# Performance work log

Measured on AMD Instinct MI355X. Metric: run time of the kernel, lower is better.

## Reference

```python
import jax, jax.numpy as jnp
import numpy as np

N_SEQ = 100_000
N_LAB = 64
E_CON = 1_600_000
D_IN = 128; D_HID = 128; BEL_OUT = 64; INC_OUT = 128
BN_EPS = 1e-5


def setup_inputs() -> dict:
    key = jax.random.key(0)
    ks = jax.random.split(key, 16)
    def W(k, i, o):
        return jax.random.normal(k, (i, o), jnp.float32) / np.float32(np.sqrt(i))
    return {
        "x_seq": jax.random.normal(ks[0], (N_SEQ, D_IN), jnp.float32),
        "x_label": jax.random.normal(ks[1], (N_LAB, D_IN), jnp.float32),
        "W1_bel": W(ks[2], D_IN, D_HID), "b1_bel": jnp.zeros((D_HID,), jnp.float32),
        "W1_inc": W(ks[3], D_IN, D_HID), "b1_inc": jnp.zeros((D_HID,), jnp.float32),
        "W1_con": W(ks[4], D_IN, D_HID), "b1_con": jnp.zeros((D_HID,), jnp.float32),
        "g1s": jnp.ones((D_HID,), jnp.float32), "beta1s": jnp.zeros((D_HID,), jnp.float32),
        "g1l": jnp.ones((D_HID,), jnp.float32), "beta1l": jnp.zeros((D_HID,), jnp.float32),
        "W2_bel": W(ks[5], D_HID, BEL_OUT), "b2_bel": jnp.zeros((BEL_OUT,), jnp.float32),
        "W2_inc": W(ks[6], D_HID, INC_OUT), "b2_inc": jnp.zeros((INC_OUT,), jnp.float32),
        "W2_con": W(ks[7], D_HID, INC_OUT), "b2_con": jnp.zeros((INC_OUT,), jnp.float32),
        "g2s": jnp.ones((INC_OUT,), jnp.float32), "beta2s": jnp.zeros((INC_OUT,), jnp.float32),
        "g2l": jnp.ones((BEL_OUT,), jnp.float32), "beta2l": jnp.zeros((BEL_OUT,), jnp.float32),
        "bel_label": jax.random.randint(ks[8], (N_SEQ,), 0, N_LAB),
        "con_src": jax.random.randint(ks[9], (E_CON,), 0, N_SEQ),
        "con_dst": jax.random.randint(ks[10], (E_CON,), 0, N_SEQ),
    }


def _inv_sqrt_deg(deg):
    # DGL norm='both': deg^{-1/2}, zero-degree nodes get 0
    return jnp.where(deg > 0, jax.lax.rsqrt(jnp.maximum(deg, 1.0)), 0.0)


def _gconv(x_src, src, dst, n_dst, W, b):
    # DGL GraphConv: y = D_dst^{-1/2} A D_src^{-1/2} x W + b
    n_src = x_src.shape[0]
    ones = jnp.ones(src.shape, x_src.dtype)
    deg_out = jax.ops.segment_sum(ones, src, num_segments=n_src)
    deg_in = jax.ops.segment_sum(ones, dst, num_segments=n_dst)
    xs = x_src * _inv_sqrt_deg(deg_out)[:, None]
    agg = jax.ops.segment_sum(xs[src], dst, num_segments=n_dst)  # [n_dst, d]
    agg = agg * _inv_sqrt_deg(deg_in)[:, None]
    return agg @ W + b


def _bn(x, g, b):
    # BatchNorm1d, training mode: biased variance, eps=1e-5
    m = jnp.mean(x, axis=0)
    v = jnp.mean(jnp.square(x - m), axis=0)
    return (x - m) * jax.lax.rsqrt(v + BN_EPS) * g + b


def _hetero_layer(h_seq, h_lab, bel_label, con_src, con_dst, Wb, bb, Wi, bi, Wc, bc):
    seq_idx = jnp.arange(h_seq.shape[0])
    # belongs_to: sequence -> label
    lab = _gconv(h_seq, seq_idx, bel_label, h_lab.shape[0], Wb, bb)
    # including: label -> sequence; connected_to: sequence -> sequence
    inc = _gconv(h_lab, bel_label, seq_idx, h_seq.shape[0], Wi, bi)
    con = _gconv(h_seq, con_src, con_dst, h_seq.shape[0], Wc, bc)
    # HeteroGraphConv aggregate='mean' over relations per dst type
    seq = 0.5 * (inc + con)
    return jax.nn.relu(seq), jax.nn.relu(lab)


def reference(x_seq, x_label,
              W1_bel, b1_bel, W1_inc, b1_inc, W1_con, b1_con,
              g1s, beta1s, g1l, beta1l,
              W2_bel, b2_bel, W2_inc, b2_inc, W2_con, b2_con,
              g2s, beta2s, g2l, beta2l,
              bel_label, con_src, con_dst):
    h_s, h_l = _hetero_layer(x_seq, x_label, bel_label, con_src, con_dst,
                             W1_bel, b1_bel, W1_inc, b1_inc, W1_con, b1_con)
    h_s = _bn(h_s, g1s, beta1s)
    h_l = _bn(h_l, g1l, beta1l)
    h_s, h_l = _hetero_layer(h_s, h_l, bel_label, con_src, con_dst,
                             W2_bel, b2_bel, W2_inc, b2_inc, W2_con, b2_con)
    h_s = _bn(h_s, g2s, beta2s)
    h_l = _bn(h_l, g2l, beta2l)
    return (h_s, h_l)
```

## Files before the change

### kernel.cpp

```cpp
#include <hip/hip_runtime.h>
#include <hip/hip_bf16.h>

#define NSEQ 100000
#define NLAB 64
#define ECON 1600000
#define D 128
#define BN_EPS 1e-5f

#define NB 196
#define BW 512
#define BCAP 10240
#define EPB 4096
#define NPART 32
#define RPB 4096

typedef unsigned int uint32;
typedef unsigned short ushort;
typedef __attribute__((ext_vector_type(8))) short bf16x8;
typedef __attribute__((ext_vector_type(4))) float f32x4;

__device__ __forceinline__ void atomAddF(float* p, float v) {
  unsafeAtomicAdd(p, v);
}
__device__ __forceinline__ float blo(uint32 u) {
  union { uint32 u; float f; } c; c.u = u << 16; return c.f;
}
__device__ __forceinline__ float bhi(uint32 u) {
  union { uint32 u; float f; } c; c.u = u & 0xFFFF0000u; return c.f;
}
__device__ __forceinline__ unsigned short f2b(float f) {
  __hip_bfloat16 h = __float2bfloat16(f);
  union { __hip_bfloat16 h; unsigned short s; } c; c.h = h; return c.s;
}

__global__ __launch_bounds__(256) void k_label_hist(const int* __restrict__ lab, int* cnt) {
  __shared__ int h[NLAB];
  if (threadIdx.x < NLAB) h[threadIdx.x] = 0;
  __syncthreads();
  for (int i = blockIdx.x * 256 + threadIdx.x; i < NSEQ; i += gridDim.x * 256)
    atomicAdd(&h[lab[i]], 1);
  __syncthreads();
  if (threadIdx.x < NLAB) atomicAdd(&cnt[threadIdx.x], h[threadIdx.x]);
}

__global__ __launch_bounds__(256) void k_binA(const int* __restrict__ src,
                                              const int* __restrict__ dst,
                                              int* bucket_cnt, int* sbucket_cnt,
                                              uint32* __restrict__ bpair,
                                              ushort* __restrict__ spair) {
  __shared__ uint32 recD[EPB];
  __shared__ ushort recS[EPB];
  __shared__ unsigned char bidD[EPB];
  __shared__ unsigned char bidS[EPB];
  __shared__ int histD[NB], histS[NB], loffD[NB], loffS[NB], gbD[NB], gbS[NB];
  int t = threadIdx.x;
  for (int i = t; i < NB; i += 256) { histD[i] = 0; histS[i] = 0; }
  __syncthreads();
  int e0 = blockIdx.x * EPB;
  int e1 = min(e0 + EPB, ECON);
  for (int e = e0 + t; e < e1; e += 256) {
    atomicAdd(&histD[dst[e] >> 9], 1);
    atomicAdd(&histS[src[e] >> 9], 1);
  }
  __syncthreads();
  if (t == 0) { int a = 0; for (int i = 0; i < NB; ++i) { loffD[i] = a; a += histD[i]; } }
  if (t == 1) { int a = 0; for (int i = 0; i < NB; ++i) { loffS[i] = a; a += histS[i]; } }
  __syncthreads();
  for (int i = t; i < NB; i += 256) {
    int c = histD[i]; gbD[i] = c ? atomicAdd(&bucket_cnt[i], c) : 0; histD[i] = 0;
    int cs = histS[i]; gbS[i] = cs ? atomicAdd(&sbucket_cnt[i], cs) : 0; histS[i] = 0;
  }
  __syncthreads();
  for (int e = e0 + t; e < e1; e += 256) {
    int s = src[e], d = dst[e];
    int b = d >> 9;
    int p = loffD[b] + atomicAdd(&histD[b], 1);
    recD[p] = (uint32)s | ((uint32)(d & (BW - 1)) << 17);
    bidD[p] = (unsigned char)b;
    int bs = s >> 9;
    int q = loffS[bs] + atomicAdd(&histS[bs], 1);
    recS[q] = (ushort)(s & (BW - 1));
    bidS[q] = (unsigned char)bs;
  }
  __syncthreads();
  int n = e1 - e0;
  for (int i = t; i < n; i += 256) {
    int b = bidD[i];
    bpair[(size_t)b * BCAP + gbD[b] + (i - loffD[b])] = recD[i];
  }
  for (int i = t; i < n; i += 256) {
    int b = bidS[i];
    spair[(size_t)b * BCAP + gbS[b] + (i - loffS[b])] = recS[i];
  }
}

__global__ __launch_bounds__(256) void k_bscan(const int* __restrict__ bucket_cnt,
                                               int* __restrict__ bbase,
                                               const int* __restrict__ cnt_lab,
                                               float* __restrict__ dinv_cnt,
                                               int* __restrict__ lab_base,
                                               int* __restrict__ lab_cursor) {
  int t = threadIdx.x;
  if (t == 0) {
    int acc = 0;
    for (int i = 0; i < NB; ++i) { bbase[i] = acc; acc += bucket_cnt[i]; }
    bbase[NB] = acc;
  }
  if (t == 1) {
    int acc = 0;
    for (int i = 0; i < NLAB; ++i) {
      lab_base[i] = acc; lab_cursor[i] = acc; acc += cnt_lab[i];
    }
    lab_base[NLAB] = acc;
  }
  if (t < NLAB) { int c = cnt_lab[t]; dinv_cnt[t] = c > 0 ? rsqrtf((float)c) : 0.f; }
}

__global__ __launch_bounds__(256) void k_binB(const uint32* __restrict__ bpair,
                                              const int* __restrict__ bucket_cnt,
                                              const int* __restrict__ bbase,
                                              int* __restrict__ off,
                                              float* __restrict__ dinv_in,
                                              int* __restrict__ esrc) {
  __shared__ int deg[BW];
  __shared__ int loff[BW];
  __shared__ int cursor[BW];
  __shared__ int wsum[4];
  int b = blockIdx.x;
  int t = threadIdx.x;
  int cnt = bucket_cnt[b];
  int gbase = bbase[b];
  const uint32* bp = &bpair[(size_t)b * BCAP];
  deg[t] = 0; deg[t + 256] = 0;
  cursor[t] = 0; cursor[t + 256] = 0;
  __syncthreads();
  for (int i = t; i < cnt; i += 256)
    atomicAdd(&deg[bp[i] >> 17], 1);
  __syncthreads();
  int d0 = deg[2 * t], d1 = deg[2 * t + 1];
  int ps = d0 + d1;
  int lane = t & 63, w = t >> 6;
  int v = ps;
  #pragma unroll
  for (int o = 1; o < 64; o <<= 1) { int n = __shfl_up(v, o); if (lane >= o) v += n; }
  if (lane == 63) wsum[w] = v;
  __syncthreads();
  int wbase = 0;
  for (int i = 0; i < w; ++i) wbase += wsum[i];
  int excl = wbase + v - ps;
  loff[2 * t] = excl;
  loff[2 * t + 1] = excl + d0;
  __syncthreads();
  #pragma unroll
  for (int k = 0; k < 2; ++k) {
    int j = t + k * 256;
    int node = b * BW + j;
    if (node < NSEQ) {
      int dg = deg[j];
      off[node] = gbase + loff[j];
      dinv_in[node] = dg > 0 ? rsqrtf((float)dg) : 0.f;
    }
  }
  if (b == NB - 1 && t == 0) off[NSEQ] = ECON;
  for (int i = t; i < cnt; i += 256) {
    uint32 pk = bp[i];
    int dl = pk >> 17;
    int p = gbase + loff[dl] + atomicAdd(&cursor[dl], 1);
    esrc[p] = (int)(pk & 0x1FFFF);
  }
}

__global__ __launch_bounds__(256) void k_binBS(const ushort* __restrict__ spair,
                                               const int* __restrict__ sbucket_cnt,
                                               float* __restrict__ dinv_out) {
  __shared__ int deg[BW];
  int b = blockIdx.x, t = threadIdx.x;
  int cnt = sbucket_cnt[b];
  deg[t] = 0; deg[t + 256] = 0;
  __syncthreads();
  const ushort* sp = &spair[(size_t)b * BCAP];
  for (int i = t; i < cnt; i += 256) atomicAdd(&deg[sp[i]], 1);
  __syncthreads();
  #pragma unroll
  for (int k = 0; k < 2; ++k) {
    int j = t + k * 256;
    int node = b * BW + j;
    if (node < NSEQ) {
      int dg = deg[j];
      dinv_out[node] = dg > 0 ? rsqrtf((float)dg) : 0.f;
    }
  }
}

__global__ __launch_bounds__(256) void k_lab_scatter(const int* __restrict__ lab,
                                                     int* lab_cursor,
                                                     int* __restrict__ lab_sorted) {
  __shared__ int hist[NLAB], base[NLAB];
  int t = threadIdx.x;
  if (t < NLAB) hist[t] = 0;
  __syncthreads();
  int r0 = blockIdx.x * RPB, r1 = min(r0 + RPB, NSEQ);
  for (int r = r0 + t; r < r1; r += 256) atomicAdd(&hist[lab[r]], 1);
  __syncthreads();
  if (t < NLAB) {
    int c = hist[t];
    base[t] = (c > 0) ? atomicAdd(&lab_cursor[t], c) : 0;
    hist[t] = 0;
  }
  __syncthreads();
  for (int r = r0 + t; r < r1; r += 256) {
    int l = lab[r];
    int p = base[l] + atomicAdd(&hist[l], 1);
    lab_sorted[p] = r;
  }
}

__global__ __launch_bounds__(256) void k_lab_agg(const uint32* __restrict__ xb,
                                                 const int* __restrict__ lab_sorted,
                                                 const int* __restrict__ lab_base,
                                                 float* __restrict__ lab_agg) {
  __shared__ float accs[4][D];
  int t = threadIdx.x;
  int l = blockIdx.x >> 3, p = blockIdx.x & 7;
  int w = t >> 6, cp = t & 63;
  int i0 = lab_base[l], i1 = lab_base[l + 1];
  float ax = 0.f, ay = 0.f;
  for (int i = i0 + p * 4 + w; i < i1; i += 32) {
    int r = lab_sorted[i];
    uint32 u = xb[r * 64 + cp];
    ax += blo(u); ay += bhi(u);
  }
  accs[w][2 * cp] = ax;
  accs[w][2 * cp + 1] = ay;
  __syncthreads();
  if (w == 0) {
    float s0 = accs[0][2 * cp] + accs[1][2 * cp] + accs[2][2 * cp] + accs[3][2 * cp];
    float s1 = accs[0][2 * cp + 1] + accs[1][2 * cp + 1] + accs[2][2 * cp + 1] + accs[3][2 * cp + 1];
    atomAddF(&lab_agg[l * D + 2 * cp], s0);
    atomAddF(&lab_agg[l * D + 2 * cp + 1], s1);
  }
}

__global__ __launch_bounds__(256) void k_cast(const float* __restrict__ x,
                                              uint32* __restrict__ xb) {
  int i = blockIdx.x * 256 + threadIdx.x;
  if (i >= NSEQ * D / 4) return;
  float4 v = ((const float4*)x)[i];
  uint32 u0 = (uint32)f2b(v.x) | ((uint32)f2b(v.y) << 16);
  uint32 u1 = (uint32)f2b(v.z) | ((uint32)f2b(v.w) << 16);
  ((uint2*)xb)[i] = make_uint2(u0, u1);
}

__global__ __launch_bounds__(256) void k_prep_w(const float* __restrict__ W1,
                                                const float* __restrict__ W2,
                                                short* __restrict__ wT1,
                                                short* __restrict__ wT2) {
  int i = blockIdx.x * 256 + threadIdx.x;
  if (i < 16384) {
    int k = i >> 7, c = i & 127;
    wT1[c * 128 + k] = (short)f2b(W1[i]);
  } else if (i < 32768) {
    int j = i - 16384;
    int k = j >> 7, c = j & 127;
    wT2[c * 128 + k] = (short)f2b(W2[j]);
  }
}

__global__ __launch_bounds__(256) void k_mm(
    const float* __restrict__ A, const float* __restrict__ rowscale,
    const float* __restrict__ W, const float* __restrict__ bias,
    float* __restrict__ out, int ncol, int relu) {
  __shared__ float sA[4 * D];
  int tid = threadIdx.x;
  int rows_pb = 256 / ncol;
  int row0 = blockIdx.x * rows_pb;
  int nload = rows_pb * D;
  for (int i = tid; i < nload; i += 256) {
    int r = row0 + (i >> 7);
    float s = rowscale ? rowscale[r] : 1.f;
    sA[i] = A[r * D + (i & 127)] * s;
  }
  __syncthreads();
  int j = tid & (ncol - 1);
  int r = tid / ncol;
  const float* a = &sA[r * D];
  const float* w = &W[j];
  float acc0 = 0.f, acc1 = 0.f, acc2 = 0.f, acc3 = 0.f;
  #pragma unroll 4
  for (int k = 0; k < D; k += 4) {
    acc0 = fmaf(a[k + 0], w[(k + 0) * ncol], acc0);
    acc1 = fmaf(a[k + 1], w[(k + 1) * ncol], acc1);
    acc2 = fmaf(a[k + 2], w[(k + 2) * ncol], acc2);
    acc3 = fmaf(a[k + 3], w[(k + 3) * ncol], acc3);
  }
  float s = (acc0 + acc1) + (acc2 + acc3);
  if (bias) s += bias[j];
  if (relu) s = fmaxf(s, 0.f);
  out[(row0 + r) * ncol + j] = s;
}

__global__ __launch_bounds__(256) void k_label_bn(
    const float* __restrict__ pre,
    const float* __restrict__ g, const float* __restrict__ beta,
    float* __restrict__ out, int ncol) {
  __shared__ float psum[256], psq[256];
  __shared__ float sa[128], sc[128];
  int tid = threadIdx.x;
  int ngrp = 256 / ncol;
  int grp = tid / ncol;
  int col = tid & (ncol - 1);
  float s = 0.f, q = 0.f;
  for (int r = grp; r < NLAB; r += ngrp) {
    float v = pre[r * ncol + col];
    s += v; q += v * v;
  }
  psum[tid] = s; psq[tid] = q;
  __syncthreads();
  if (tid < ncol) {
    float S = 0.f, Q = 0.f;
    for (int gi = 0; gi < ngrp; ++gi) { S += psum[gi * ncol + tid]; Q += psq[gi * ncol + tid]; }
    float m = S * (1.f / NLAB);
    float v = Q * (1.f / NLAB) - m * m;
    float a = rsqrtf(v + BN_EPS) * g[tid];
    sa[tid] = a; sc[tid] = beta[tid] - m * a;
  }
  __syncthreads();
  for (int i = tid; i < NLAB * ncol; i += 256) {
    int c = i & (ncol - 1);
    out[i] = pre[i] * sa[c] + sc[c];
  }
}

__global__ __launch_bounds__(256) void k_con_agg_bf(
    const uint32* __restrict__ xb, const int* __restrict__ esrc,
    const int* __restrict__ off,
    const float* __restrict__ dinv_out, const float* __restrict__ dinv_in,
    uint32* __restrict__ outb) {
  int wid = (blockIdx.x * 256 + threadIdx.x) >> 6;
  int lane = threadIdx.x & 63;
  if (wid >= NSEQ) return;
  int e0 = off[wid], e1 = off[wid + 1];
  float ax = 0.f, ay = 0.f;
  int e = e0;
  for (; e + 3 < e1; e += 4) {
    int s0 = esrc[e], s1 = esrc[e + 1], s2 = esrc[e + 2], s3 = esrc[e + 3];
    float w0 = dinv_out[s0], w1 = dinv_out[s1], w2 = dinv_out[s2], w3 = dinv_out[s3];
    uint32 u0 = xb[s0 * 64 + lane];
    uint32 u1 = xb[s1 * 64 + lane];
    uint32 u2 = xb[s2 * 64 + lane];
    uint32 u3 = xb[s3 * 64 + lane];
    ax += blo(u0) * w0 + blo(u1) * w1 + blo(u2) * w2 + blo(u3) * w3;
    ay += bhi(u0) * w0 + bhi(u1) * w1 + bhi(u2) * w2 + bhi(u3) * w3;
  }
  for (; e < e1; ++e) {
    int s0 = esrc[e];
    float w0 = dinv_out[s0];
    uint32 u0 = xb[s0 * 64 + lane];
    ax += blo(u0) * w0;
    ay += bhi(u0) * w0;
  }
  float di = dinv_in[wid];
  uint32 p = (uint32)f2b(ax * di) | ((uint32)f2b(ay * di) << 16);
  outb[wid * 64 + lane] = p;
}

template <int OUTBF>
__global__ __launch_bounds__(256) void k_gemm_mfma(
    const short* __restrict__ aggbf,
    const short* __restrict__ wT,
    const float* __restrict__ b_con,
    const float* __restrict__ y_inc,
    const float* __restrict__ b_inc,
    const float* __restrict__ dinv_cnt,
    const int* __restrict__ bel,
    float* __restrict__ outF,
    short* __restrict__ outB,
    float* __restrict__ statsP) {
  __shared__ short sW[128 * 136];
  __shared__ float csum[D], csq[D];
  int t = threadIdx.x;
  {
    const uint4* src = (const uint4*)wT;
    for (int i = t; i < 2048; i += 256) {
      int row = i >> 4, part = i & 15;
      *(uint4*)&sW[row * 136 + part * 8] = src[i];
    }
  }
  if (t < D) { csum[t] = 0.f; csq[t] = 0.f; }
  int w = t >> 6, l = t & 63;
  int lr = l & 15, lg = l >> 4;
  int row0 = blockIdx.x * 64 + w * 16;
  bf16x8 afrag[4];
  {
    int arow = min(row0 + lr, NSEQ - 1);
    const short* ab = aggbf + arow * 128 + lg * 8;
    #pragma unroll
    for (int kt = 0; kt < 4; ++kt)
      afrag[kt] = *(const bf16x8*)(ab + kt * 32);
  }
  __syncthreads();
  f32x4 acc[8];
  #pragma unroll
  for (int ct = 0; ct < 8; ++ct) {
    f32x4 a = {0.f, 0.f, 0.f, 0.f};
    const short* wb = &sW[(ct * 16 + lr) * 136 + lg * 8];
    #pragma unroll
    for (int kt = 0; kt < 4; ++kt) {
      bf16x8 bfr = *(const bf16x8*)(wb + kt * 32);
      a = __builtin_amdgcn_mfma_f32_16x16x32_bf16(afrag[kt], bfr, a, 0, 0, 0);
    }
    acc[ct] = a;
  }
  int belr[4]; float dcv[4]; int rowv[4];
  #pragma unroll
  for (int r = 0; r < 4; ++r) {
    int gr = row0 + lg * 4 + r;
    rowv[r] = gr;
    int cl = min(gr, NSEQ - 1);
    belr[r] = bel[cl];
    dcv[r] = dinv_cnt[belr[r]];
  }
  #pragma unroll
  for (int ct = 0; ct < 8; ++ct) {
    int col = ct * 16 + lr;
    float bc = b_con[col], bi = b_inc[col];
    float s = 0.f, q = 0.f;
    #pragma unroll
    for (int r = 0; r < 4; ++r) {
      if (rowv[r] < NSEQ) {
        float o = acc[ct][r] + bc + fmaf(dcv[r], y_inc[belr[r] * D + col], bi);
        o = fmaxf(0.5f * o, 0.f);
        if (OUTBF) outB[rowv[r] * D + col] = (short)f2b(o);
        else       outF[rowv[r] * D + col] = o;
        s += o; q += o * o;
      }
    }
    s += __shfl_xor(s, 16); s += __shfl_xor(s, 32);
    q += __shfl_xor(q, 16); q += __shfl_xor(q, 32);
    if (lg == 0) {
      atomicAdd(&csum[col], s);
      atomicAdd(&csq[col], q);
    }
  }
  __syncthreads();
  float* sp = statsP + (blockIdx.x & (NPART - 1)) * 256;
  if (t < D) {
    atomAddF(&sp[t], csum[t]);
    atomAddF(&sp[D + t], csq[t]);
  }
}

__global__ __launch_bounds__(256) void k_bn_apply_bf(
    const uint32* __restrict__ pre, const float* __restrict__ statsP,
    const float* __restrict__ g, const float* __restrict__ beta,
    uint32* __restrict__ xb) {
  int t = threadIdx.x;
  int w = t >> 6, cp = t & 63;
  int c0 = 2 * cp, c1 = 2 * cp + 1;
  float s0 = 0.f, q0 = 0.f, s1 = 0.f, q1 = 0.f;
  #pragma unroll
  for (int k = 0; k < NPART; ++k) {
    const float* sp = statsP + k * 256;
    s0 += sp[c0]; q0 += sp[128 + c0];
    s1 += sp[c1]; q1 += sp[128 + c1];
  }
  const float invN = 1.f / (float)NSEQ;
  float m0 = s0 * invN, m1 = s1 * invN;
  float a0 = rsqrtf(q0 * invN - m0 * m0 + BN_EPS) * g[c0];
  float a1 = rsqrtf(q1 * invN - m1 * m1 + BN_EPS) * g[c1];
  float cc0 = beta[c0] - m0 * a0;
  float cc1 = beta[c1] - m1 * a1;
  for (int r = blockIdx.x * 4 + w; r < NSEQ; r += gridDim.x * 4) {
    uint32 u = pre[r * 64 + cp];
    float v0 = blo(u) * a0 + cc0;
    float v1 = bhi(u) * a1 + cc1;
    xb[r * 64 + cp] = (uint32)f2b(v0) | ((uint32)f2b(v1) << 16);
  }
}

__global__ __launch_bounds__(256) void k_bn_apply2(
    float* __restrict__ buf, const float* __restrict__ statsP,
    const float* __restrict__ g, const float* __restrict__ beta) {
  int t = threadIdx.x;
  int w = t >> 6, cp = t & 63;
  int c0 = 2 * cp, c1 = 2 * cp + 1;
  float s0 = 0.f, q0 = 0.f, s1 = 0.f, q1 = 0.f;
  #pragma unroll
  for (int k = 0; k < NPART; ++k) {
    const float* sp = statsP + k * 256;
    s0 += sp[c0]; q0 += sp[128 + c0];
    s1 += sp[c1]; q1 += sp[128 + c1];
  }
  const float invN = 1.f / (float)NSEQ;
  float m0 = s0 * invN, m1 = s1 * invN;
  float a0 = rsqrtf(q0 * invN - m0 * m0 + BN_EPS) * g[c0];
  float a1 = rsqrtf(q1 * invN - m1 * m1 + BN_EPS) * g[c1];
  float cc0 = beta[c0] - m0 * a0;
  float cc1 = beta[c1] - m1 * a1;
  for (int r = blockIdx.x * 4 + w; r < NSEQ; r += gridDim.x * 4) {
    float2 v = ((float2*)buf)[r * 64 + cp];
    v.x = v.x * a0 + cc0;
    v.y = v.y * a1 + cc1;
    ((float2*)buf)[r * 64 + cp] = v;
  }
}

extern "C" void kernel_launch(void* const* d_in, const int* in_sizes, int n_in,
                              void* d_out, int out_size, void* d_ws, size_t ws_size,
                              hipStream_t stream) {
  const float* x_seq   = (const float*)d_in[0];
  const float* x_label = (const float*)d_in[1];
  const float* W1_bel  = (const float*)d_in[2];
  const float* b1_bel  = (const float*)d_in[3];
  const float* W1_inc  = (const float*)d_in[4];
  const float* b1_inc  = (const float*)d_in[5];
  const float* W1_con  = (const float*)d_in[6];
  const float* b1_con  = (const float*)d_in[7];
  const float* g1s     = (const float*)d_in[8];
  const float* beta1s  = (const float*)d_in[9];
  const float* g1l     = (const float*)d_in[10];
  const float* beta1l  = (const float*)d_in[11];
  const float* W2_bel  = (const float*)d_in[12];
  const float* b2_bel  = (const float*)d_in[13];
  const float* W2_inc  = (const float*)d_in[14];
  const float* b2_inc  = (const float*)d_in[15];
  const float* W2_con  = (const float*)d_in[16];
  const float* b2_con  = (const float*)d_in[17];
  const float* g2s     = (const float*)d_in[18];
  const float* beta2s  = (const float*)d_in[19];
  const float* g2l     = (const float*)d_in[20];
  const float* beta2l  = (const float*)d_in[21];
  const int* bel       = (const int*)d_in[22];
  const int* con_src   = (const int*)d_in[23];
  const int* con_dst   = (const int*)d_in[24];
  float* out = (float*)d_out;

  char* ws = (char*)d_ws;
  short*  aggbf    = (short*) (ws);
  short*  h1pre    = (short*) (ws + 25600000);
  uint32* bpair    = (uint32*)(ws + 32000000);
  ushort* spair    = (ushort*)(ws + 40028160);
  int*    esrc     = (int*)   (ws + 51200000);
  float*  dinv_out = (float*) (ws + 57600000);
  int*    cnt_lab     = (int*)  (ws + 58000000);
  int*    bucket_cnt  = (int*)  (ws + 58001024);
  int*    sbucket_cnt = (int*)  (ws + 58002048);
  float*  statsP1     = (float*)(ws + 58003072);
  float*  statsP2     = (float*)(ws + 58035840);
  float*  lab_agg1    = (float*)(ws + 58068608);
  float*  lab_agg2    = (float*)(ws + 58101376);
  float*  dinv_in    = (float*)(ws + 58134144);
  float*  dinv_cnt   = (float*)(ws + 58534144);
  int*    bbase      = (int*)  (ws + 58534400);
  int*    off        = (int*)  (ws + 58535424);
  float*  y_inc1     = (float*)(ws + 58935552);
  float*  y_inc2     = (float*)(ws + 58968320);
  float*  h_l1       = (float*)(ws + 59001088);
  short*  wT1        = (short*)(ws + 59033856);
  short*  wT2        = (short*)(ws + 59066624);
  int*    lab_base   = (int*)  (ws + 59099392);
  int*    lab_cursor = (int*)  (ws + 59100416);
  int*    lab_sorted = (int*)  (ws + 59101440);

  uint32* xb = (uint32*)out;
  float* belp1 = (float*)ws;
  float* belp2 = (float*)ws;

  hipMemsetAsync(ws + 58000000, 0, 134144, stream);

  k_label_hist <<<256, 256, 0, stream>>>(bel, cnt_lab);
  k_binA       <<<(ECON + EPB - 1) / EPB, 256, 0, stream>>>(con_src, con_dst,
                                                            bucket_cnt, sbucket_cnt,
                                                            bpair, spair);
  k_bscan      <<<1, 256, 0, stream>>>(bucket_cnt, bbase, cnt_lab, dinv_cnt,
                                       lab_base, lab_cursor);
  k_binB       <<<NB, 256, 0, stream>>>(bpair, bucket_cnt, bbase,
                                        off, dinv_in, esrc);
  k_binBS      <<<NB, 256, 0, stream>>>(spair, sbucket_cnt, dinv_out);
  k_lab_scatter<<<(NSEQ + RPB - 1) / RPB, 256, 0, stream>>>(bel, lab_cursor, lab_sorted);
  k_cast       <<<(NSEQ * D / 4 + 255) / 256, 256, 0, stream>>>(x_seq, xb);
  k_prep_w     <<<128, 256, 0, stream>>>(W1_con, W2_con, wT1, wT2);

  k_lab_agg    <<<NLAB * 8, 256, 0, stream>>>(xb, lab_sorted, lab_base, lab_agg1);
  k_mm         <<<32, 256, 0, stream>>>(x_label, nullptr, W1_inc, nullptr, y_inc1, 128, 0);
  k_mm         <<<32, 256, 0, stream>>>(lab_agg1, dinv_cnt, W1_bel, b1_bel, belp1, 128, 1);
  k_label_bn   <<<1, 256, 0, stream>>>(belp1, g1l, beta1l, h_l1, 128);
  k_con_agg_bf <<<NSEQ / 4, 256, 0, stream>>>(xb, esrc, off, dinv_out, dinv_in,
                                              (uint32*)aggbf);
  k_gemm_mfma<1><<<(NSEQ + 63) / 64, 256, 0, stream>>>(
                   aggbf, wT1, b1_con, y_inc1, b1_inc, dinv_cnt, bel,
                   nullptr, h1pre, statsP1);
  k_bn_apply_bf<<<1024, 256, 0, stream>>>((uint32*)h1pre, statsP1, g1s, beta1s, xb);

  k_lab_agg    <<<NLAB * 8, 256, 0, stream>>>(xb, lab_sorted, lab_base, lab_agg2);
  k_mm         <<<32, 256, 0, stream>>>(h_l1, nullptr, W2_inc, nullptr, y_inc2, 128, 0);
  k_mm         <<<16, 256, 0, stream>>>(lab_agg2, dinv_cnt, W2_bel, b2_bel, belp2, 64, 1);
  k_label_bn   <<<1, 256, 0, stream>>>(belp2, g2l, beta2l, out + (size_t)NSEQ * D, 64);
  k_con_agg_bf <<<NSEQ / 4, 256, 0, stream>>>(xb, esrc, off, dinv_out, dinv_in,
                                              (uint32*)aggbf);
  k_gemm_mfma<0><<<(NSEQ + 63) / 64, 256, 0, stream>>>(
                   aggbf, wT2, b2_con, y_inc2, b2_inc, dinv_cnt, bel,
                   out, nullptr, statsP2);
  k_bn_apply2  <<<1024, 256, 0, stream>>>(out, statsP2, g2s, beta2s);
}
```

Before: 455.8 us.

## Fold layer-1 BatchNorm affine into layer-2 aggregation kernels

Drops the separate pass that applied the first BatchNorm to all sequence rows. The per-channel scale and shift are now computed once in a tiny kernel and folded algebraically into the layer-2 label aggregation and edge aggregation: the scale multiplies the summed features, and the shift is added weighted by the edge-weight sum or the row count. This removes a full read and write of the 100k x 128 bf16 activation, at the cost of an extra per-edge weight accumulation and a small parameter kernel. The final BN apply now reads precomputed parameters instead of reducing the partial stats in every block.

Result: faster. 433.6 us (median of 2 runs) (-4.9%).

```diff
diff --git a/kernel.cpp b/kernel.cpp
--- a/kernel.cpp
+++ b/kernel.cpp
@@ -215,9 +215,31 @@
   }
 }
 
+__global__ __launch_bounds__(128) void k_bnparams(const float* __restrict__ statsP,
+                                                  const float* __restrict__ g,
+                                                  const float* __restrict__ beta,
+                                                  float* __restrict__ aV,
+                                                  float* __restrict__ ccV) {
+  int c = threadIdx.x;
+  float s = 0.f, q = 0.f;
+  #pragma unroll
+  for (int k = 0; k < NPART; ++k) {
+    s += statsP[k * 256 + c];
+    q += statsP[k * 256 + 128 + c];
+  }
+  const float invN = 1.f / (float)NSEQ;
+  float m = s * invN;
+  float a = rsqrtf(q * invN - m * m + BN_EPS) * g[c];
+  aV[c] = a;
+  ccV[c] = beta[c] - m * a;
+}
+
+template <int AFFINE>
 __global__ __launch_bounds__(256) void k_lab_agg(const uint32* __restrict__ xb,
                                                  const int* __restrict__ lab_sorted,
                                                  const int* __restrict__ lab_base,
+                                                 const float* __restrict__ aV,
+                                                 const float* __restrict__ ccV,
                                                  float* __restrict__ lab_agg) {
   __shared__ float accs[4][D];
   int t = threadIdx.x;
@@ -236,6 +258,15 @@
   if (w == 0) {
     float s0 = accs[0][2 * cp] + accs[1][2 * cp] + accs[2][2 * cp] + accs[3][2 * cp];
     float s1 = accs[0][2 * cp + 1] + accs[1][2 * cp + 1] + accs[2][2 * cp + 1] + accs[3][2 * cp + 1];
+    if (AFFINE) {
+      s0 *= aV[2 * cp];
+      s1 *= aV[2 * cp + 1];
+      if (p == 0) {
+        float cnt = (float)(i1 - i0);
+        s0 += cnt * ccV[2 * cp];
+        s1 += cnt * ccV[2 * cp + 1];
+      }
+    }
     atomAddF(&lab_agg[l * D + 2 * cp], s0);
     atomAddF(&lab_agg[l * D + 2 * cp + 1], s1);
   }
@@ -331,16 +362,18 @@
   }
 }
 
+template <int AFFINE>
 __global__ __launch_bounds__(256) void k_con_agg_bf(
     const uint32* __restrict__ xb, const int* __restrict__ esrc,
     const int* __restrict__ off,
     const float* __restrict__ dinv_out, const float* __restrict__ dinv_in,
+    const float* __restrict__ aV, const float* __restrict__ ccV,
     uint32* __restrict__ outb) {
   int wid = (blockIdx.x * 256 + threadIdx.x) >> 6;
   int lane = threadIdx.x & 63;
   if (wid >= NSEQ) return;
   int e0 = off[wid], e1 = off[wid + 1];
-  float ax = 0.f, ay = 0.f;
+  float ax = 0.f, ay = 0.f, sw = 0.f;
   int e = e0;
   for (; e + 3 < e1; e += 4) {
     int s0 = esrc[e], s1 = esrc[e + 1], s2 = esrc[e + 2], s3 = esrc[e + 3];
@@ -351,6 +384,7 @@
     uint32 u3 = xb[s3 * 64 + lane];
     ax += blo(u0) * w0 + blo(u1) * w1 + blo(u2) * w2 + blo(u3) * w3;
     ay += bhi(u0) * w0 + bhi(u1) * w1 + bhi(u2) * w2 + bhi(u3) * w3;
+    if (AFFINE) sw += (w0 + w1) + (w2 + w3);
   }
   for (; e < e1; ++e) {
     int s0 = esrc[e];
@@ -358,9 +392,20 @@
     uint32 u0 = xb[s0 * 64 + lane];
     ax += blo(u0) * w0;
     ay += bhi(u0) * w0;
+    if (AFFINE) sw += w0;
   }
   float di = dinv_in[wid];
-  uint32 p = (uint32)f2b(ax * di) | ((uint32)f2b(ay * di) << 16);
+  float rx, ry;
+  if (AFFINE) {
+    float a0 = aV[2 * lane], a1 = aV[2 * lane + 1];
+    float c0 = ccV[2 * lane], c1 = ccV[2 * lane + 1];
+    rx = di * fmaf(a0, ax, c0 * sw);
+    ry = di * fmaf(a1, ay, c1 * sw);
+  } else {
+    rx = di * ax;
+    ry = di * ay;
+  }
+  uint32 p = (uint32)f2b(rx) | ((uint32)f2b(ry) << 16);
   outb[wid * 64 + lane] = p;
 }
 
@@ -450,57 +495,17 @@
   }
 }
 
-__global__ __launch_bounds__(256) void k_bn_apply_bf(
-    const uint32* __restrict__ pre, const float* __restrict__ statsP,
-    const float* __restrict__ g, const float* __restrict__ beta,
-    uint32* __restrict__ xb) {
+__global__ __launch_bounds__(256) void k_bn_apply2(
+    float* __restrict__ buf, const float* __restrict__ aV,
+    const float* __restrict__ ccV) {
   int t = threadIdx.x;
   int w = t >> 6, cp = t & 63;
-  int c0 = 2 * cp, c1 = 2 * cp + 1;
-  float s0 = 0.f, q0 = 0.f, s1 = 0.f, q1 = 0.f;
-  #pragma unroll
-  for (int k = 0; k < NPART; ++k) {
-    const float* sp = statsP + k * 256;
-    s0 += sp[c0]; q0 += sp[128 + c0];
-    s1 += sp[c1]; q1 += sp[128 + c1];
-  }
-  const float invN = 1.f / (float)NSEQ;
-  float m0 = s0 * invN, m1 = s1 * invN;
-  float a0 = rsqrtf(q0 * invN - m0 * m0 + BN_EPS) * g[c0];
-  float a1 = rsqrtf(q1 * invN - m1 * m1 + BN_EPS) * g[c1];
-  float cc0 = beta[c0] - m0 * a0;
-  float cc1 = beta[c1] - m1 * a1;
-  for (int r = blockIdx.x * 4 + w; r < NSEQ; r += gridDim.x * 4) {
-    uint32 u = pre[r * 64 + cp];
-    float v0 = blo(u) * a0 + cc0;
-    float v1 = bhi(u) * a1 + cc1;
-    xb[r * 64 + cp] = (uint32)f2b(v0) | ((uint32)f2b(v1) << 16);
-  }
-}
-
-__global__ __launch_bounds__(256) void k_bn_apply2(
-    float* __restrict__ buf, const float* __restrict__ statsP,
-    const float* __restrict__ g, const float* __restrict__ beta) {
-  int t = threadIdx.x;
-  int w = t >> 6, cp = t & 63;
-  int c0 = 2 * cp, c1 = 2 * cp + 1;
-  float s0 = 0.f, q0 = 0.f, s1 = 0.f, q1 = 0.f;
-  #pragma unroll
-  for (int k = 0; k < NPART; ++k) {
-    const float* sp = statsP + k * 256;
-    s0 += sp[c0]; q0 += sp[128 + c0];
-    s1 += sp[c1]; q1 += sp[128 + c1];
-  }
-  const float invN = 1.f / (float)NSEQ;
-  float m0 = s0 * invN, m1 = s1 * invN;
-  float a0 = rsqrtf(q0 * invN - m0 * m0 + BN_EPS) * g[c0];
-  float a1 = rsqrtf(q1 * invN - m1 * m1 + BN_EPS) * g[c1];
-  float cc0 = beta[c0] - m0 * a0;
-  float cc1 = beta[c1] - m1 * a1;
+  float a0 = aV[2 * cp], a1 = aV[2 * cp + 1];
+  float c0 = ccV[2 * cp], c1 = ccV[2 * cp + 1];
   for (int r = blockIdx.x * 4 + w; r < NSEQ; r += gridDim.x * 4) {
     float2 v = ((float2*)buf)[r * 64 + cp];
-    v.x = v.x * a0 + cc0;
-    v.y = v.y * a1 + cc1;
+    v.x = fmaf(v.x, a0, c0);
+    v.y = fmaf(v.y, a1, c1);
     ((float2*)buf)[r * 64 + cp] = v;
   }
 }
@@ -561,6 +566,10 @@
   int*    lab_base   = (int*)  (ws + 59099392);
   int*    lab_cursor = (int*)  (ws + 59100416);
   int*    lab_sorted = (int*)  (ws + 59101440);
+  float*  ab1        = (float*)(ws + 59501440);
+  float*  cc1        = (float*)(ws + 59501952);
+  float*  ab2        = (float*)(ws + 59502464);
+  float*  cc2        = (float*)(ws + 59502976);
 
   uint32* xb = (uint32*)out;
   float* belp1 = (float*)ws;
@@ -581,25 +590,29 @@
   k_cast       <<<(NSEQ * D / 4 + 255) / 256, 256, 0, stream>>>(x_seq, xb);
   k_prep_w     <<<128, 256, 0, stream>>>(W1_con, W2_con, wT1, wT2);
 
-  k_lab_agg    <<<NLAB * 8, 256, 0, stream>>>(xb, lab_sorted, lab_base, lab_agg1);
+  k_lab_agg<0> <<<NLAB * 8, 256, 0, stream>>>(xb, lab_sorted, lab_base,
+                                              nullptr, nullptr, lab_agg1);
   k_mm         <<<32, 256, 0, stream>>>(x_label, nullptr, W1_inc, nullptr, y_inc1, 128, 0);
   k_mm         <<<32, 256, 0, stream>>>(lab_agg1, dinv_cnt, W1_bel, b1_bel, belp1, 128, 1);
   k_label_bn   <<<1, 256, 0, stream>>>(belp1, g1l, beta1l, h_l1, 128);
-  k_con_agg_bf <<<NSEQ / 4, 256, 0, stream>>>(xb, esrc, off, dinv_out, dinv_in,
-                                              (uint32*)aggbf);
+  k_con_agg_bf<0><<<NSEQ / 4, 256, 0, stream>>>(xb, esrc, off, dinv_out, dinv_in,
+                                                nullptr, nullptr, (uint32*)aggbf);
   k_gemm_mfma<1><<<(NSEQ + 63) / 64, 256, 0, stream>>>(
                    aggbf, wT1, b1_con, y_inc1, b1_inc, dinv_cnt, bel,
                    nullptr, h1pre, statsP1);
-  k_bn_apply_bf<<<1024, 256, 0, stream>>>((uint32*)h1pre, statsP1, g1s, beta1s, xb);
-
-  k_lab_agg    <<<NLAB * 8, 256, 0, stream>>>(xb, lab_sorted, lab_base, lab_agg2);
+  k_bnparams   <<<1, 128, 0, stream>>>(statsP1, g1s, beta1s, ab1, cc1);
+
+  k_lab_agg<1> <<<NLAB * 8, 256, 0, stream>>>((const uint32*)h1pre, lab_sorted,
+                                              lab_base, ab1, cc1, lab_agg2);
   k_mm         <<<32, 256, 0, stream>>>(h_l1, nullptr, W2_inc, nullptr, y_inc2, 128, 0);
   k_mm         <<<16, 256, 0, stream>>>(lab_agg2, dinv_cnt, W2_bel, b2_bel, belp2, 64, 1);
   k_label_bn   <<<1, 256, 0, stream>>>(belp2, g2l, beta2l, out + (size_t)NSEQ * D, 64);
-  k_con_agg_bf <<<NSEQ / 4, 256, 0, stream>>>(xb, esrc, off, dinv_out, dinv_in,
-                                              (uint32*)aggbf);
+  k_con_agg_bf<1><<<NSEQ / 4, 256, 0, stream>>>((const uint32*)h1pre, esrc, off,
+                                                dinv_out, dinv_in, ab1, cc1,
+                                                (uint32*)aggbf);
   k_gemm_mfma<0><<<(NSEQ + 63) / 64, 256, 0, stream>>>(
                    aggbf, wT2, b2_con, y_inc2, b2_inc, dinv_cnt, bel,
                    out, nullptr, statsP2);
-  k_bn_apply2  <<<1024, 256, 0, stream>>>(out, statsP2, g2s, beta2s);
-}
+  k_bnparams   <<<1, 128, 0, stream>>>(statsP2, g2s, beta2s, ab2, cc2);
+  k_bn_apply2  <<<1024, 256, 0, stream>>>(out, ab2, cc2);
+}
```
